# Optimization experiments

Hardware: AMD Instinct MI355X
Metric: run time of the kernel (lower is better)

## Reference

```python
import jax, jax.numpy as jnp
import numpy as np

N_WIRES = 4
N_OPS = 20

# Deterministic surrogate for tq.RandomLayer(n_ops=20): fixed random op list.
_rng = np.random.default_rng(1234)
OPS = []
for _i in range(N_OPS):
    kind = ['rx', 'ry', 'rz', 'cnot'][int(_rng.integers(4))]
    w = int(_rng.integers(N_WIRES))
    OPS.append((kind, w))

C64 = jnp.complex64

def _ry(theta):
    c = jnp.cos(theta / 2).astype(C64)
    s = jnp.sin(theta / 2).astype(C64)
    return jnp.stack([jnp.stack([c, -s], -1), jnp.stack([s, c], -1)], -2)

def _rx(theta):
    c = jnp.cos(theta / 2).astype(C64)
    s = jnp.sin(theta / 2).astype(C64)
    return jnp.stack([jnp.stack([c, -1j * s], -1), jnp.stack([-1j * s, c], -1)], -2)

def _rz(theta):
    e0 = jnp.exp(-1j * theta.astype(C64) / 2)
    e1 = jnp.exp(1j * theta.astype(C64) / 2)
    z = jnp.zeros_like(e0)
    return jnp.stack([jnp.stack([e0, z], -1), jnp.stack([z, e1], -1)], -2)

_CNOT = jnp.array([[1, 0, 0, 0], [0, 1, 0, 0], [0, 0, 0, 1], [0, 0, 1, 0]],
                  dtype=C64).reshape(2, 2, 2, 2)

def _apply_1q(state, gate, w):
    # state: (N,2,2,2,2); gate: (2,2) or (N,2,2)
    s = jnp.moveaxis(state, 1 + w, -1)
    if gate.ndim == 2:
        s = jnp.einsum('ij,n...j->n...i', gate, s)
    else:
        s = jnp.einsum('nij,n...j->n...i', gate, s)
    return jnp.moveaxis(s, -1, 1 + w)

def _apply_2q(state, gate4, c, t):
    s = jnp.moveaxis(state, (1 + c, 1 + t), (-2, -1))
    s = jnp.einsum('abcd,n...cd->n...ab', gate4, s)
    return jnp.moveaxis(s, (-2, -1), (1 + c, 1 + t))

def quantum_layer(vec, rand_angles, rx_theta, ry_theta):
    # vec: (N, 4) real angles. Returns (N, 4) PauliZ expectations.
    n = vec.shape[0]
    state = jnp.zeros((n, 2 ** N_WIRES), C64).at[:, 0].set(1.0)
    state = state.reshape((n,) + (2,) * N_WIRES)
    # GeneralEncoder '4xRy': RY(vec[:, w]) on each wire (batched angles)
    for w in range(N_WIRES):
        state = _apply_1q(state, _ry(vec[:, w]), w)
    # RandomLayer surrogate
    for i, (kind, w) in enumerate(OPS):
        th = rand_angles[i]
        if kind == 'rx':
            state = _apply_1q(state, _rx(th), w)
        elif kind == 'ry':
            state = _apply_1q(state, _ry(th), w)
        elif kind == 'rz':
            state = _apply_1q(state, _rz(th), w)
        else:
            state = _apply_2q(state, _CNOT, w, (w + 1) % N_WIRES)
    # Trainable RX/RY (single shared param each), applied on every wire
    gx, gy = _rx(rx_theta), _ry(ry_theta)
    for w in range(N_WIRES):
        state = _apply_1q(state, gx, w)
        state = _apply_1q(state, gy, w)
    # MeasureAll PauliZ
    probs = state.real ** 2 + state.imag ** 2  # (N,2,2,2,2)
    zs = []
    for w in range(N_WIRES):
        axes = tuple(a for a in range(1, 1 + N_WIRES) if a != 1 + w)
        m = probs.sum(axis=axes)  # (N, 2)
        zs.append(m[:, 0] - m[:, 1])
    return jnp.stack(zs, -1)

def _apply_quantum(t, rand_angles, rx_theta, ry_theta):
    # t: (B, H, T, D) -> elementwise per-(b,h,t) quantum transform
    B, H, T, D = t.shape
    out = quantum_layer(t.reshape(B * H * T, D), rand_angles, rx_theta, ry_theta)
    return out.reshape(B, H, T, D)

def setup_inputs() -> dict:
    key = jax.random.key(0)
    ks = jax.random.split(key, 7)
    B, T, C = 4, 2048, 256
    H, D = 64, 4
    x = jax.random.normal(ks[0], (B, T, C), jnp.float32)
    w_qkv = jax.random.normal(ks[1], (3 * C, C), jnp.float32) * (1.0 / np.sqrt(C))
    w_out = jax.random.normal(ks[2], (C, C), jnp.float32) * (1.0 / np.sqrt(C))
    b_out = jnp.zeros((C,), jnp.float32)
    rx_theta = jax.random.uniform(ks[3], (), jnp.float32, 0.0, 2 * np.pi)
    ry_theta = jax.random.uniform(ks[4], (), jnp.float32, 0.0, 2 * np.pi)
    rand_angles = jax.random.uniform(ks[5], (N_OPS,), jnp.float32, 0.0, 2 * np.pi)
    return {'x': x, 'w_qkv': w_qkv, 'w_out': w_out, 'b_out': b_out,
            'rx_theta': rx_theta, 'ry_theta': ry_theta, 'rand_angles': rand_angles}

def reference(x, w_qkv, w_out, b_out, rx_theta, ry_theta, rand_angles):
    B, T, C = x.shape
    H, D = 64, 4
    qkv = (x @ w_qkv.T).reshape(B, T, 3, H, D).transpose(2, 0, 3, 1, 4)
    q, k, v = qkv[0], qkv[1], qkv[2]  # each (B, H, T, D)
    q = _apply_quantum(q, rand_angles, rx_theta, ry_theta)
    k = _apply_quantum(k, rand_angles, rx_theta, ry_theta)
    v = _apply_quantum(v, rand_angles, rx_theta, ry_theta)
    # Faithful to original einsum labels: q,k,v are (B,H,T,D) so 't','s' index heads
    scores = jnp.einsum('bthd,bshd->bths', q, k) / (D ** 0.5)  # (B,H,T,H)
    attn = jax.nn.softmax(scores, axis=-1)  # dropout is eval-mode identity
    out = jnp.einsum('bths,bshd->bthd', attn, v)  # (B,H,T,D)
    out = out.reshape(B, T, C)  # faithful memory-layout reshape as in original
    return out @ w_out.T + b_out
```

## Files before the change

### kernel.cpp

```cpp
#include <hip/hip_runtime.h>
#include <stdint.h>
#include <stddef.h>

typedef __attribute__((ext_vector_type(8))) short short8;
typedef __attribute__((ext_vector_type(4))) float floatx4;

static void compute_ops_host(int* kinds, int* wires) {
  const uint32_t MULT_A = 0x931e8875u;
  const uint32_t INIT_B = 0x8b51f9ddu, MULT_B = 0x58f38dedu;
  const uint32_t MIX_L = 0xca01f9ddu, MIX_R = 0x4973f715u;
  uint32_t hc = 0x43b0d7e5u;
  auto hashmix = [&](uint32_t v) -> uint32_t {
    v ^= hc; hc *= MULT_A; v *= hc; v ^= v >> 16; return v;
  };
  auto mix = [&](uint32_t x, uint32_t y) -> uint32_t {
    uint32_t r = (x * MIX_L) - (y * MIX_R); r ^= r >> 16; return r;
  };
  uint32_t pool[4];
  for (int i = 0; i < 4; ++i) pool[i] = hashmix(i == 0 ? 1234u : 0u);
  for (int s = 0; s < 4; ++s)
    for (int d = 0; d < 4; ++d)
      if (s != d) pool[d] = mix(pool[d], hashmix(pool[s]));
  uint32_t st32[8];
  uint32_t hcb = INIT_B;
  for (int i = 0; i < 8; ++i) {
    uint32_t dv = pool[i & 3];
    dv ^= hcb; hcb *= MULT_B; dv *= hcb; dv ^= dv >> 16;
    st32[i] = dv;
  }
  uint64_t s64[4];
  for (int k = 0; k < 4; ++k) s64[k] = (uint64_t)st32[2 * k] | ((uint64_t)st32[2 * k + 1] << 32);
  const __uint128_t M = ((__uint128_t)0x2360ed051fc65da4ULL << 64) | 0x4385df649fccf645ULL;
  __uint128_t initstate = ((__uint128_t)s64[0] << 64) | s64[1];
  __uint128_t inc = ((((__uint128_t)s64[2] << 64) | s64[3]) << 1) | (__uint128_t)1;
  __uint128_t state = inc;
  state += initstate;
  state = state * M + inc;
  bool has = false; uint32_t hbuf = 0;
  auto next32 = [&]() -> uint32_t {
    if (has) { has = false; return hbuf; }
    state = state * M + inc;
    uint64_t hi = (uint64_t)(state >> 64), lo = (uint64_t)state;
    uint64_t x = hi ^ lo;
    unsigned rot = (unsigned)(state >> 122) & 63u;
    uint64_t o = (x >> rot) | (x << ((64u - rot) & 63u));
    has = true; hbuf = (uint32_t)(o >> 32);
    return (uint32_t)o;
  };
  for (int i = 0; i < 20; ++i) {
    kinds[i] = (int)(((uint64_t)next32() * 4ull) >> 32);
    wires[i] = (int)(((uint64_t)next32() * 4ull) >> 32);
  }
}

__global__ __launch_bounds__(256) void build_tables(
    const float* __restrict__ rand_angles, const float* __restrict__ rx_theta,
    const float* __restrict__ ry_theta, unsigned long long kinds,
    unsigned long long wires, float* __restrict__ Tg)
{
  __shared__ float Ur[16][16], Ui[16][16];
  __shared__ float Msh[4][16][16];
  const int tid = threadIdx.x;
  {
    int i = tid >> 4, j = tid & 15;
    Ur[i][j] = (i == j) ? 1.0f : 0.0f;
    Ui[i][j] = 0.0f;
  }
  __syncthreads();
  for (int g = 0; g < 28; ++g) {
    int kind, w; float th;
    if (g < 20) {
      kind = (int)((kinds >> (2 * g)) & 3ull);
      w = (int)((wires >> (2 * g)) & 3ull);
      th = rand_angles[g];
    } else {
      int e = g - 20;
      w = e >> 1;
      kind = (e & 1) ? 1 : 0;
      th = (e & 1) ? ry_theta[0] : rx_theta[0];
    }
    if (kind == 3) {
      int mc = 8 >> w, mt = 8 >> ((w + 1) & 3);
      if (tid < 64) {
        int pi = tid >> 4, j = tid & 15;
        int i = mc, pbit = 0;
        for (int b = 3; b >= 0; --b) {
          int mask = 1 << b;
          if (mask != mc && mask != mt) { i |= ((pi >> pbit) & 1) << b; pbit++; }
        }
        int i2 = i | mt;
        float tr = Ur[i][j], ti = Ui[i][j];
        Ur[i][j] = Ur[i2][j]; Ui[i][j] = Ui[i2][j];
        Ur[i2][j] = tr; Ui[i2][j] = ti;
      }
    } else {
      float s, c;
      sincosf(th * 0.5f, &s, &c);
      float g00r, g00i, g01r, g01i, g10r, g10i, g11r, g11i;
      if (kind == 0) {
        g00r = c; g00i = 0; g01r = 0; g01i = -s; g10r = 0; g10i = -s; g11r = c; g11i = 0;
      } else if (kind == 1) {
        g00r = c; g00i = 0; g01r = -s; g01i = 0; g10r = s; g10i = 0; g11r = c; g11i = 0;
      } else {
        g00r = c; g00i = -s; g01r = 0; g01i = 0; g10r = 0; g10i = 0; g11r = c; g11i = s;
      }
      if (tid < 128) {
        int p = tid >> 4, j = tid & 15;
        int mb = 3 - w;
        int i0 = ((p >> mb) << (mb + 1)) | (p & ((1 << mb) - 1));
        int i1 = i0 | (1 << mb);
        float ar = Ur[i0][j], ai = Ui[i0][j];
        float br = Ur[i1][j], bi = Ui[i1][j];
        Ur[i0][j] = g00r * ar - g00i * ai + g01r * br - g01i * bi;
        Ui[i0][j] = g00r * ai + g00i * ar + g01r * bi + g01i * br;
        Ur[i1][j] = g10r * ar - g10i * ai + g11r * br - g11i * bi;
        Ui[i1][j] = g10r * ai + g10i * ar + g11r * bi + g11i * br;
      }
    }
    __syncthreads();
  }
  {
    int j = tid >> 4, k = tid & 15;
    float m0 = 0, m1 = 0, m2 = 0, m3 = 0;
#pragma unroll
    for (int l = 0; l < 16; ++l) {
      float p = Ur[l][j] * Ur[l][k] + Ui[l][j] * Ui[l][k];
      m0 += (l & 8) ? -p : p;
      m1 += (l & 4) ? -p : p;
      m2 += (l & 2) ? -p : p;
      m3 += (l & 1) ? -p : p;
    }
    Msh[0][j][k] = m0; Msh[1][j][k] = m1; Msh[2][j][k] = m2; Msh[3][j][k] = m3;
  }
  __syncthreads();
  if (tid < 81) {
    int e4 = tid % 3, r = tid / 3;
    int ee0 = r / 9, ee1 = (r / 3) % 3, ee2 = r % 3;
    int ee[4] = { ee0, ee1, ee2, e4 };
    float s0 = 0, s1 = 0, s2 = 0, s3 = 0;
    for (int m = 0; m < 16; ++m) {
      int j = 0, k = 0; float coef = 1.0f;
      for (int i = 0; i < 4; ++i) {
        int o = (m >> i) & 1;
        int e = ee[i];
        int bj, bk; float c;
        if (e == 2)      { bj = o; bk = 1 - o; c = 0.5f; }
        else if (e == 1) { bj = o; bk = o;     c = o ? -0.5f : 0.5f; }
        else             { bj = o; bk = o;     c = 0.5f; }
        j |= bj << (3 - i); k |= bk << (3 - i);
        coef *= c;
      }
      s0 += coef * Msh[0][j][k]; s1 += coef * Msh[1][j][k];
      s2 += coef * Msh[2][j][k]; s3 += coef * Msh[3][j][k];
    }
    Tg[(0 * 27 + r) * 4 + e4] = s0;
    Tg[(1 * 27 + r) * 4 + e4] = s1;
    Tg[(2 * 27 + r) * 4 + e4] = s2;
    Tg[(3 * 27 + r) * 4 + e4] = s3;
  }
  if (tid >= 81 && tid < 108) {
    int r = tid - 81;
    for (int w = 0; w < 4; ++w) Tg[(w * 27 + r) * 4 + 3] = 0.0f;
  }
}

static __device__ __forceinline__ unsigned short bf16_rn(float x) {
  uint32_t u = __float_as_uint(x);
  return (unsigned short)((u + 0x7FFFu + ((u >> 16) & 1u)) >> 16);
}
static __device__ __forceinline__ void split2(float x, unsigned short& h, unsigned short& l) {
  h = bf16_rn(x);
  float hf = __uint_as_float(((uint32_t)h) << 16);
  l = bf16_rn(x - hf);
}

__global__ __launch_bounds__(256) void conv_split(
    const float* __restrict__ in, unsigned short* __restrict__ h,
    unsigned short* __restrict__ l, int n4)
{
  int i = blockIdx.x * 256 + threadIdx.x;
  if (i >= n4) return;
  float4 v = *reinterpret_cast<const float4*>(&in[(size_t)i * 4]);
  ushort4 hh, ll;
  split2(v.x, hh.x, ll.x);
  split2(v.y, hh.y, ll.y);
  split2(v.z, hh.z, ll.z);
  split2(v.w, hh.w, ll.w);
  *reinterpret_cast<ushort4*>(&h[(size_t)i * 4]) = hh;
  *reinterpret_cast<ushort4*>(&l[(size_t)i * 4]) = ll;
}

__global__ __launch_bounds__(256) void gemm_mfma_split(
    const unsigned short* __restrict__ Ah, const unsigned short* __restrict__ Al,
    const unsigned short* __restrict__ Bh, const unsigned short* __restrict__ Bl,
    const float* __restrict__ bias, float* __restrict__ C,
    int M, int N, int K)
{
  __shared__ __align__(16) unsigned short sAh[128 * 32];
  __shared__ __align__(16) unsigned short sAl[128 * 32];
  __shared__ __align__(16) unsigned short sBh[64 * 32];
  __shared__ __align__(16) unsigned short sBl[64 * 32];
  const int tid = threadIdx.x;
  const int bm = blockIdx.y * 128, bn = blockIdx.x * 64;
  const int wave = tid >> 6, lane = tid & 63;
  const int wm = wave >> 1, wn = wave & 1;
  const int fr = lane & 15, fg = lane >> 4;
  floatx4 acc[4][2] = {};
  for (int k0 = 0; k0 < K; k0 += 32) {
    __syncthreads();
#pragma unroll
    for (int rd = 0; rd < 2; ++rd) {
      int q = tid + rd * 256;
      int r = q >> 2, c8 = (q & 3) * 8;
      size_t go = (size_t)(bm + r) * K + (k0 + c8);
      *reinterpret_cast<uint4*>(&sAh[q * 8]) = *reinterpret_cast<const uint4*>(&Ah[go]);
      *reinterpret_cast<uint4*>(&sAl[q * 8]) = *reinterpret_cast<const uint4*>(&Al[go]);
    }
    {
      int r = tid >> 2, c8 = (tid & 3) * 8;
      size_t go = (size_t)(bn + r) * K + (k0 + c8);
      *reinterpret_cast<uint4*>(&sBh[tid * 8]) = *reinterpret_cast<const uint4*>(&Bh[go]);
      *reinterpret_cast<uint4*>(&sBl[tid * 8]) = *reinterpret_cast<const uint4*>(&Bl[go]);
    }
    __syncthreads();
    short8 a_h[4], a_l[4], b_h[2], b_l[2];
#pragma unroll
    for (int fm = 0; fm < 4; ++fm) {
      int row = wm * 64 + fm * 16 + fr;
      a_h[fm] = *reinterpret_cast<const short8*>(&sAh[row * 32 + fg * 8]);
      a_l[fm] = *reinterpret_cast<const short8*>(&sAl[row * 32 + fg * 8]);
    }
#pragma unroll
    for (int fn = 0; fn < 2; ++fn) {
      int row = wn * 32 + fn * 16 + fr;
      b_h[fn] = *reinterpret_cast<const short8*>(&sBh[row * 32 + fg * 8]);
      b_l[fn] = *reinterpret_cast<const short8*>(&sBl[row * 32 + fg * 8]);
    }
#pragma unroll
    for (int fm = 0; fm < 4; ++fm)
#pragma unroll
      for (int fn = 0; fn < 2; ++fn) {
        acc[fm][fn] = __builtin_amdgcn_mfma_f32_16x16x32_bf16(a_h[fm], b_h[fn], acc[fm][fn], 0, 0, 0);
        acc[fm][fn] = __builtin_amdgcn_mfma_f32_16x16x32_bf16(a_h[fm], b_l[fn], acc[fm][fn], 0, 0, 0);
        acc[fm][fn] = __builtin_amdgcn_mfma_f32_16x16x32_bf16(a_l[fm], b_h[fn], acc[fm][fn], 0, 0, 0);
      }
  }
#pragma unroll
  for (int fm = 0; fm < 4; ++fm) {
    int rowb = bm + wm * 64 + fm * 16 + fg * 4;
#pragma unroll
    for (int fn = 0; fn < 2; ++fn) {
      int col = bn + wn * 32 + fn * 16 + fr;
      float bv = (bias != nullptr) ? bias[col] : 0.0f;
#pragma unroll
      for (int r = 0; r < 4; ++r)
        C[(size_t)(rowb + r) * N + col] = acc[fm][fn][r] + bv;
    }
  }
}

__global__ __launch_bounds__(256) void quantum_apply1(
    float* __restrict__ p0, const float* __restrict__ Tg)
{
  size_t base = ((size_t)blockIdx.x * 256 + threadIdx.x) * 4;
  float4 A = *reinterpret_cast<const float4*>(&p0[base]);
  float cv[4], sv[4];
  __sincosf(A.x, &sv[0], &cv[0]);
  __sincosf(A.y, &sv[1], &cv[1]);
  __sincosf(A.z, &sv[2], &cv[2]);
  __sincosf(A.w, &sv[3], &cv[3]);
  float z[4];
#pragma unroll
  for (int w = 0; w < 4; ++w) {
    float a1_ = 0.f;
#pragma unroll
    for (int e1 = 0; e1 < 3; ++e1) {
      float a2_ = 0.f;
#pragma unroll
      for (int e2 = 0; e2 < 3; ++e2) {
        float a3_ = 0.f;
#pragma unroll
        for (int e3 = 0; e3 < 3; ++e3) {
          const float4 t4 = *reinterpret_cast<const float4*>(
              &Tg[(w * 27 + e1 * 9 + e2 * 3 + e3) * 4]);
          float inner = fmaf(sv[3], t4.z, fmaf(cv[3], t4.y, t4.x));
          if (e3 == 0)      a3_ += inner;
          else if (e3 == 1) a3_ = fmaf(inner, cv[2], a3_);
          else              a3_ = fmaf(inner, sv[2], a3_);
        }
        if (e2 == 0)      a2_ += a3_;
        else if (e2 == 1) a2_ = fmaf(a3_, cv[1], a2_);
        else              a2_ = fmaf(a3_, sv[1], a2_);
      }
      if (e1 == 0)      a1_ += a2_;
      else if (e1 == 1) a1_ = fmaf(a2_, cv[0], a1_);
      else              a1_ = fmaf(a2_, sv[0], a1_);
    }
    z[w] = a1_;
  }
  *reinterpret_cast<float4*>(&p0[base]) = make_float4(z[0], z[1], z[2], z[3]);
}

__global__ __launch_bounds__(256) void attn64b(
    const float* __restrict__ qkv, unsigned short* __restrict__ yh,
    unsigned short* __restrict__ yl)
{
  __shared__ float Ksh[4][64][4];
  __shared__ float Vsh[4][64][4];
  const int wave = threadIdx.x >> 6, lane = threadIdx.x & 63;
  const int posIdx = blockIdx.x * 4 + wave;
  const float* row = qkv + (size_t)posIdx * 768;
  float4 q = *reinterpret_cast<const float4*>(&row[lane * 4]);
  *reinterpret_cast<float4*>(&Ksh[wave][lane][0]) =
      *reinterpret_cast<const float4*>(&row[256 + lane * 4]);
  *reinterpret_cast<float4*>(&Vsh[wave][lane][0]) =
      *reinterpret_cast<const float4*>(&row[512 + lane * 4]);
  __syncthreads();
  float nx = 0, ny = 0, nz = 0, nw = 0, den = 0;
#pragma unroll
  for (int ss = 0; ss < 64; ++ss) {
    float d = q.x * Ksh[wave][ss][0] + q.y * Ksh[wave][ss][1] +
              q.z * Ksh[wave][ss][2] + q.w * Ksh[wave][ss][3];
    float e = __expf(d * 0.5f);
    den += e;
    nx = fmaf(e, Vsh[wave][ss][0], nx);
    ny = fmaf(e, Vsh[wave][ss][1], ny);
    nz = fmaf(e, Vsh[wave][ss][2], nz);
    nw = fmaf(e, Vsh[wave][ss][3], nw);
  }
  float inv = 1.0f / den;
  const int b = posIdx >> 11, pos = posIdx & 2047;
  size_t off = (((size_t)(b * 64 + lane)) * 2048 + pos) * 4;
  ushort4 hh, ll;
  split2(nx * inv, hh.x, ll.x);
  split2(ny * inv, hh.y, ll.y);
  split2(nz * inv, hh.z, ll.z);
  split2(nw * inv, hh.w, ll.w);
  *reinterpret_cast<ushort4*>(&yh[off]) = hh;
  *reinterpret_cast<ushort4*>(&yl[off]) = ll;
}

extern "C" void kernel_launch(void* const* d_in, const int* in_sizes, int n_in,
                              void* d_out, int out_size, void* d_ws, size_t ws_size,
                              hipStream_t stream)
{
  const float* x    = (const float*)d_in[0];
  const float* wqkv = (const float*)d_in[1];
  const float* wout = (const float*)d_in[2];
  const float* bout = (const float*)d_in[3];
  const float* rxth = (const float*)d_in[4];
  const float* ryth = (const float*)d_in[5];
  const float* rang = (const float*)d_in[6];
  float* out = (float*)d_out;

  uint8_t* w8 = (uint8_t*)d_ws;
  float* Tg = (float*)w8;
  float* p0 = (float*)(w8 + 4096);
  uint8_t* bb = w8 + 4096 + (size_t)8192 * 768 * 4;
  unsigned short* xh  = (unsigned short*)bb;
  unsigned short* xl  = xh + (size_t)8192 * 256;
  unsigned short* wh  = xl + (size_t)8192 * 256;
  unsigned short* wl  = wh + (size_t)768 * 256;
  unsigned short* woh = wl + (size_t)768 * 256;
  unsigned short* wol = woh + (size_t)256 * 256;
  unsigned short* yh  = wol + (size_t)256 * 256;
  unsigned short* yl  = yh + (size_t)8192 * 256;

  int kinds[20], wires[20];
  compute_ops_host(kinds, wires);
  unsigned long long pk = 0, pw = 0;
  for (int i = 0; i < 20; ++i) {
    pk |= (unsigned long long)(kinds[i] & 3) << (2 * i);
    pw |= (unsigned long long)(wires[i] & 3) << (2 * i);
  }

  hipLaunchKernelGGL(build_tables, dim3(1), dim3(256), 0, stream,
                     rang, rxth, ryth, pk, pw, Tg);
  hipLaunchKernelGGL(conv_split, dim3(2048), dim3(256), 0, stream, x, xh, xl, 524288);
  hipLaunchKernelGGL(conv_split, dim3(192), dim3(256), 0, stream, wqkv, wh, wl, 49152);
  hipLaunchKernelGGL(conv_split, dim3(64), dim3(256), 0, stream, wout, woh, wol, 16384);
  hipLaunchKernelGGL(gemm_mfma_split, dim3(12, 64), dim3(256), 0, stream,
                     xh, xl, wh, wl, (const float*)nullptr, p0, 8192, 768, 256);
  hipLaunchKernelGGL(quantum_apply1, dim3(6144), dim3(256), 0, stream, p0, Tg);
  hipLaunchKernelGGL(attn64b, dim3(2048), dim3(256), 0, stream, p0, yh, yl);
  hipLaunchKernelGGL(gemm_mfma_split, dim3(4, 64), dim3(256), 0, stream,
                     yh, yl, woh, wol, bout, out, 8192, 256, 256);
}
```

Before: 96.29 us.

## Fuse bf16 split into GEMM loads and quantum circuit into attention kernel

The three standalone fp32-to-bf16 hi/lo split kernels are removed. The GEMM now loads fp32 tiles and splits them while staging into shared memory, and the attention kernel writes fp32 output instead of split bf16. The quantum-circuit evaluation is folded into the attention kernel, removing a read-modify-write pass over the qkv buffer and one launch. The cost is that the split is redone per tile, since each A row block is converted for every N-block column and each weight tile for every M-block, and the GEMM global loads double in size because they are fp32.

```diff
diff --git a/kernel.cpp b/kernel.cpp
--- a/kernel.cpp
+++ b/kernel.cpp
@@ -3,6 +3,7 @@
 #include <stddef.h>
 
 typedef __attribute__((ext_vector_type(8))) short short8;
+typedef __attribute__((ext_vector_type(8))) unsigned short ushort8v;
 typedef __attribute__((ext_vector_type(4))) float floatx4;
 
 static void compute_ops_host(int* kinds, int* wires) {
@@ -173,26 +174,22 @@
   float hf = __uint_as_float(((uint32_t)h) << 16);
   l = bf16_rn(x - hf);
 }
-
-__global__ __launch_bounds__(256) void conv_split(
-    const float* __restrict__ in, unsigned short* __restrict__ h,
-    unsigned short* __restrict__ l, int n4)
-{
-  int i = blockIdx.x * 256 + threadIdx.x;
-  if (i >= n4) return;
-  float4 v = *reinterpret_cast<const float4*>(&in[(size_t)i * 4]);
-  ushort4 hh, ll;
-  split2(v.x, hh.x, ll.x);
-  split2(v.y, hh.y, ll.y);
-  split2(v.z, hh.z, ll.z);
-  split2(v.w, hh.w, ll.w);
-  *reinterpret_cast<ushort4*>(&h[(size_t)i * 4]) = hh;
-  *reinterpret_cast<ushort4*>(&l[(size_t)i * 4]) = ll;
-}
-
-__global__ __launch_bounds__(256) void gemm_mfma_split(
-    const unsigned short* __restrict__ Ah, const unsigned short* __restrict__ Al,
-    const unsigned short* __restrict__ Bh, const unsigned short* __restrict__ Bl,
+static __device__ __forceinline__ void split8_store(
+    float4 fa, float4 fb, unsigned short* dsth, unsigned short* dstl) {
+  float v[8] = { fa.x, fa.y, fa.z, fa.w, fb.x, fb.y, fb.z, fb.w };
+  ushort8v hh, ll;
+#pragma unroll
+  for (int i = 0; i < 8; ++i) {
+    unsigned short h, l;
+    split2(v[i], h, l);
+    hh[i] = h; ll[i] = l;
+  }
+  *reinterpret_cast<ushort8v*>(dsth) = hh;
+  *reinterpret_cast<ushort8v*>(dstl) = ll;
+}
+
+__global__ __launch_bounds__(256) void gemm_a32(
+    const float* __restrict__ A, const float* __restrict__ B,
     const float* __restrict__ bias, float* __restrict__ C,
     int M, int N, int K)
 {
@@ -212,15 +209,17 @@
     for (int rd = 0; rd < 2; ++rd) {
       int q = tid + rd * 256;
       int r = q >> 2, c8 = (q & 3) * 8;
-      size_t go = (size_t)(bm + r) * K + (k0 + c8);
-      *reinterpret_cast<uint4*>(&sAh[q * 8]) = *reinterpret_cast<const uint4*>(&Ah[go]);
-      *reinterpret_cast<uint4*>(&sAl[q * 8]) = *reinterpret_cast<const uint4*>(&Al[go]);
+      const float* src = &A[(size_t)(bm + r) * K + (k0 + c8)];
+      float4 fa = *reinterpret_cast<const float4*>(src);
+      float4 fb = *reinterpret_cast<const float4*>(src + 4);
+      split8_store(fa, fb, &sAh[q * 8], &sAl[q * 8]);
     }
     {
       int r = tid >> 2, c8 = (tid & 3) * 8;
-      size_t go = (size_t)(bn + r) * K + (k0 + c8);
-      *reinterpret_cast<uint4*>(&sBh[tid * 8]) = *reinterpret_cast<const uint4*>(&Bh[go]);
-      *reinterpret_cast<uint4*>(&sBl[tid * 8]) = *reinterpret_cast<const uint4*>(&Bl[go]);
+      const float* src = &B[(size_t)(bn + r) * K + (k0 + c8)];
+      float4 fa = *reinterpret_cast<const float4*>(src);
+      float4 fb = *reinterpret_cast<const float4*>(src + 4);
+      split8_store(fa, fb, &sBh[tid * 8], &sBl[tid * 8]);
     }
     __syncthreads();
     short8 a_h[4], a_l[4], b_h[2], b_l[2];
@@ -259,11 +258,9 @@
   }
 }
 
-__global__ __launch_bounds__(256) void quantum_apply1(
-    float* __restrict__ p0, const float* __restrict__ Tg)
-{
-  size_t base = ((size_t)blockIdx.x * 256 + threadIdx.x) * 4;
-  float4 A = *reinterpret_cast<const float4*>(&p0[base]);
+static __device__ __forceinline__ float4 quantum_vec(
+    const float* __restrict__ Tg, float4 A)
+{
   float cv[4], sv[4];
   __sincosf(A.x, &sv[0], &cv[0]);
   __sincosf(A.y, &sv[1], &cv[1]);
@@ -298,23 +295,26 @@
     }
     z[w] = a1_;
   }
-  *reinterpret_cast<float4*>(&p0[base]) = make_float4(z[0], z[1], z[2], z[3]);
-}
-
-__global__ __launch_bounds__(256) void attn64b(
-    const float* __restrict__ qkv, unsigned short* __restrict__ yh,
-    unsigned short* __restrict__ yl)
+  return make_float4(z[0], z[1], z[2], z[3]);
+}
+
+__global__ __launch_bounds__(256) void attn_q(
+    const float* __restrict__ qkv, const float* __restrict__ Tg,
+    float* __restrict__ y)
 {
   __shared__ float Ksh[4][64][4];
   __shared__ float Vsh[4][64][4];
   const int wave = threadIdx.x >> 6, lane = threadIdx.x & 63;
   const int posIdx = blockIdx.x * 4 + wave;
   const float* row = qkv + (size_t)posIdx * 768;
-  float4 q = *reinterpret_cast<const float4*>(&row[lane * 4]);
-  *reinterpret_cast<float4*>(&Ksh[wave][lane][0]) =
-      *reinterpret_cast<const float4*>(&row[256 + lane * 4]);
-  *reinterpret_cast<float4*>(&Vsh[wave][lane][0]) =
-      *reinterpret_cast<const float4*>(&row[512 + lane * 4]);
+  float4 qa = *reinterpret_cast<const float4*>(&row[lane * 4]);
+  float4 ka = *reinterpret_cast<const float4*>(&row[256 + lane * 4]);
+  float4 va = *reinterpret_cast<const float4*>(&row[512 + lane * 4]);
+  float4 q = quantum_vec(Tg, qa);
+  float4 k = quantum_vec(Tg, ka);
+  float4 v = quantum_vec(Tg, va);
+  *reinterpret_cast<float4*>(&Ksh[wave][lane][0]) = k;
+  *reinterpret_cast<float4*>(&Vsh[wave][lane][0]) = v;
   __syncthreads();
   float nx = 0, ny = 0, nz = 0, nw = 0, den = 0;
 #pragma unroll
@@ -330,14 +330,8 @@
   }
   float inv = 1.0f / den;
   const int b = posIdx >> 11, pos = posIdx & 2047;
-  size_t off = (((size_t)(b * 64 + lane)) * 2048 + pos) * 4;
-  ushort4 hh, ll;
-  split2(nx * inv, hh.x, ll.x);
-  split2(ny * inv, hh.y, ll.y);
-  split2(nz * inv, hh.z, ll.z);
-  split2(nw * inv, hh.w, ll.w);
-  *reinterpret_cast<ushort4*>(&yh[off]) = hh;
-  *reinterpret_cast<ushort4*>(&yl[off]) = ll;
+  *reinterpret_cast<float4*>(&y[(((size_t)(b * 64 + lane)) * 2048 + pos) * 4]) =
+      make_float4(nx * inv, ny * inv, nz * inv, nw * inv);
 }
 
 extern "C" void kernel_launch(void* const* d_in, const int* in_sizes, int n_in,
@@ -356,15 +350,7 @@
   uint8_t* w8 = (uint8_t*)d_ws;
   float* Tg = (float*)w8;
   float* p0 = (float*)(w8 + 4096);
-  uint8_t* bb = w8 + 4096 + (size_t)8192 * 768 * 4;
-  unsigned short* xh  = (unsigned short*)bb;
-  unsigned short* xl  = xh + (size_t)8192 * 256;
-  unsigned short* wh  = xl + (size_t)8192 * 256;
-  unsigned short* wl  = wh + (size_t)768 * 256;
-  unsigned short* woh = wl + (size_t)768 * 256;
-  unsigned short* wol = woh + (size_t)256 * 256;
-  unsigned short* yh  = wol + (size_t)256 * 256;
-  unsigned short* yl  = yh + (size_t)8192 * 256;
+  float* y  = p0 + (size_t)8192 * 768;
 
   int kinds[20], wires[20];
   compute_ops_host(kinds, wires);
@@ -376,13 +362,9 @@
 
   hipLaunchKernelGGL(build_tables, dim3(1), dim3(256), 0, stream,
                      rang, rxth, ryth, pk, pw, Tg);
-  hipLaunchKernelGGL(conv_split, dim3(2048), dim3(256), 0, stream, x, xh, xl, 524288);
-  hipLaunchKernelGGL(conv_split, dim3(192), dim3(256), 0, stream, wqkv, wh, wl, 49152);
-  hipLaunchKernelGGL(conv_split, dim3(64), dim3(256), 0, stream, wout, woh, wol, 16384);
-  hipLaunchKernelGGL(gemm_mfma_split, dim3(12, 64), dim3(256), 0, stream,
-                     xh, xl, wh, wl, (const float*)nullptr, p0, 8192, 768, 256);
-  hipLaunchKernelGGL(quantum_apply1, dim3(6144), dim3(256), 0, stream, p0, Tg);
-  hipLaunchKernelGGL(attn64b, dim3(2048), dim3(256), 0, stream, p0, yh, yl);
-  hipLaunchKernelGGL(gemm_mfma_split, dim3(4, 64), dim3(256), 0, stream,
-                     yh, yl, woh, wol, bout, out, 8192, 256, 256);
-}
+  hipLaunchKernelGGL(gemm_a32, dim3(12, 64), dim3(256), 0, stream,
+                     x, wqkv, (const float*)nullptr, p0, 8192, 768, 256);
+  hipLaunchKernelGGL(attn_q, dim3(2048), dim3(256), 0, stream, p0, Tg, y);
+  hipLaunchKernelGGL(gemm_a32, dim3(4, 64), dim3(256), 0, stream,
+                     y, wout, bout, out, 8192, 256, 256);
+}
```

After: 95.77 us. Within noise of the previous version (-0.5%).
